# Performance work log

Measured on AMD Instinct MI355X. Metric: run time of the kernel, lower is better.

## Reference

```python
import jax, jax.numpy as jnp
import numpy as np

# ---- constants mirroring init_kwargs ----
S = 128          # sheet_units
KA = 25          # aff_cf_units
C = 2            # aff_cf_channels
KL = 25          # lat_cf_units
EXC = 9          # exc_units
DA = 1           # aff_cf_dilation
DL = 1           # lat_cf_dilation
HOMEO_TARGET = 0.04
STRENGTH = 1.0

# ---- radial helper masks (get_circle / get_radial_cos) ----
def _dist(n):
    g = jnp.arange(n, dtype=jnp.float32) - (n - 1) / 2.0
    return jnp.sqrt(g[:, None] ** 2 + g[None, :] ** 2)

def _circle(n, r):
    return (_dist(n) < r).astype(jnp.float32)

def _rcos(n, wl):
    return jnp.cos(_dist(n) * jnp.pi / wl)

# afferent envelope: [C*KA*KA], channel-major like torch repeat+view
_ae = _rcos(KA, KA) ** 2 * _circle(KA, KA / 2)
_ae = _ae / _ae.max()
AFF_ENV = jnp.tile(_ae.reshape(1, KA * KA), (C, 1)).reshape(C * KA * KA)

# lateral (LRI) envelope: [KL*KL]
_inh = _rcos(KL, EXC / DL) ** 2 * _circle(KL, EXC / (2 * DL))
_le = _rcos(KL, KL) ** 2 * (1.0 - _inh) * _circle(KL, KL / 2)
LRI_ENV = (_le / _le.max()).reshape(KL * KL)

def _unfold(x, k, dil):
    """x: [C,H,W] -> patches [L, C*k*k], torch F.unfold ordering (C slowest)."""
    Cc, H, W = x.shape
    out = H - dil * (k - 1)
    idx = jnp.arange(out)[:, None] + dil * jnp.arange(k)[None, :]  # [out,k]
    p = x[:, idx, :]          # [C,out,k,W]
    p = p[:, :, :, idx]       # [C,out,k,out,k]
    p = p.transpose(1, 3, 0, 2, 4)  # [out_i,out_j,C,ki,kj]
    return p.reshape(out * out, Cc * k * k)

def setup_inputs() -> dict:
    key = jax.random.key(0)
    k1, k2 = jax.random.split(key)
    in_size = S + DA * (KA - 1)  # 152
    x = jax.random.uniform(k1, (1, C, in_size, in_size), dtype=jnp.float32)
    rfs = jax.random.uniform(k2, (S * S, C * KA * KA, 1), dtype=jnp.float32)
    rfs = rfs / rfs.sum(1, keepdims=True)
    lat_weights = jnp.ones((S * S, KL * KL, 1), jnp.float32) / (KL * KL)
    adathresh = jnp.zeros((1, 1, S, S), jnp.float32)
    return {"x": x, "rfs": rfs, "lat_weights": lat_weights, "adathresh": adathresh}

def _forward(x, rfs, lat_weights, adathresh):
    relu = jax.nn.relu
    rfs = relu(rfs)                 # no_grad positive clamp of params
    lw = relu(lat_weights)
    # afferent: unfold + envelope + per-pixel dot (bmm with [L,F,1])
    tiles = _unfold(x[0], KA, DA) * AFF_ENV[None, :]          # [L, C*KA*KA]
    raw_aff = jnp.einsum('lf,lf->l', tiles, rfs[:, :, 0]).reshape(S, S)
    aff = jax.lax.stop_gradient(raw_aff) - adathresh[0, 0]
    lat = relu(aff)
    # lateral inhibition: pad so unfold yields S*S positions
    p = DL * (KL - 1) // 2
    lt = _unfold(jnp.pad(lat, p)[None], KL, DL) * LRI_ENV[None, :]  # [L, KL*KL]
    lat_neg = jnp.einsum('lf,lf->l', lt, jax.lax.stop_gradient(lw)[:, :, 0]).reshape(S, S)
    lat = lat - lat_neg
    lat = jnp.tanh(relu(lat * STRENGTH + aff))
    # hebbian lateral correlations term (learning_flag path)
    lt2 = _unfold(jnp.pad(lat, p, constant_values=HOMEO_TARGET)[None], KL, DL) * LRI_ENV[None, :]
    weighted = lt2 * lat.reshape(S * S, 1)
    lat_correlations = jnp.einsum('lf,lf->', weighted, lw[:, :, 0])
    return (raw_aff.reshape(1, 1, S, S), lat.reshape(1, 1, S, S),
            lat_correlations, tiles[:, None, :])

def reference(x, rfs, lat_weights, adathresh):
    return _forward(x, rfs, lat_weights, adathresh)
```

## Files before the change

kernel.cpp:

```cpp
#include <hip/hip_runtime.h>
#include <math.h>

#define S 128
#define KA 25
#define KL 25
#define PATCH (KA * KA)
#define FEAT (2 * PATCH)
#define PI_F 3.14159265358979323846f

#define WS_ENV 0
#define WS_LAT0 640
#define WS_PART 17024

__global__ __launch_bounds__(256) void k_tiles_aff(const float* __restrict__ x,
                                                   const float* __restrict__ rfs,
                                                   const float* __restrict__ ada,
                                                   float* __restrict__ raw_aff,
                                                   float* __restrict__ tiles,
                                                   float* __restrict__ ws) {
    __shared__ float s_ae[PATCH];
    __shared__ float s_part[4];
    const int tid = threadIdx.x;
    const int lane = tid & 63;
    const int wv = tid >> 6;

    for (int i = tid; i < PATCH; i += 256) {
        float di = (float)(i / KA) - 12.0f;
        float dj = (float)(i % KA) - 12.0f;
        float d = sqrtf(di * di + dj * dj);
        float v = 0.0f;
        if (d < 12.5f) {
            float c = cosf(d * (PI_F / 25.0f));
            v = c * c;
        }
        s_ae[i] = v;
    }
    __syncthreads();

    const int l = blockIdx.x;
    const int li = l >> 7;
    const int lj = l & 127;
    const long base = (long)l * FEAT;

    float acc = 0.0f;
    for (int f = tid; f < FEAT; f += 256) {
        int c = (f >= PATCH) ? 1 : 0;
        int r = f - c * PATCH;
        int ki = r / KA;
        int kj = r - ki * KA;
        float xv = x[c * (152 * 152) + (li + ki) * 152 + (lj + kj)];
        float t = xv * s_ae[r];
        tiles[base + f] = t;
        acc += t * fmaxf(rfs[base + f], 0.0f);
    }

    for (int off = 32; off > 0; off >>= 1) acc += __shfl_down(acc, off);
    if (lane == 0) s_part[wv] = acc;
    __syncthreads();
    if (tid == 0) {
        float ra = s_part[0] + s_part[1] + s_part[2] + s_part[3];
        raw_aff[l] = ra;
        ws[WS_LAT0 + l] = fmaxf(ra - ada[l], 0.0f);
    }

    if (blockIdx.x == 0) {
        __syncthreads();
        float m = 0.0f;
        for (int i = tid; i < PATCH; i += 256) {
            float di = (float)(i / KL) - 12.0f;
            float dj = (float)(i % KL) - 12.0f;
            float d = sqrtf(di * di + dj * dj);
            float v = 0.0f;
            if (d < 12.5f) {
                float c1 = cosf(d * (PI_F / 25.0f));
                float inh = 0.0f;
                if (d < 4.5f) {
                    float c2 = cosf(d * (PI_F / 9.0f));
                    inh = c2 * c2;
                }
                v = c1 * c1 * (1.0f - inh);
            }
            s_ae[i] = v;
            m = fmaxf(m, v);
        }
        for (int off = 32; off > 0; off >>= 1) m = fmaxf(m, __shfl_down(m, off));
        if (lane == 0) s_part[wv] = m;
        __syncthreads();
        float inv = 1.0f / fmaxf(fmaxf(s_part[0], s_part[1]),
                                 fmaxf(s_part[2], s_part[3]));
        for (int i = tid; i < PATCH; i += 256) ws[WS_ENV + i] = s_ae[i] * inv;
    }
}

__global__ __launch_bounds__(256) void k_lat(const float* __restrict__ raw_aff,
                                             const float* __restrict__ ada,
                                             const float* __restrict__ lw,
                                             float* __restrict__ latf,
                                             const float* __restrict__ ws) {
    __shared__ float s_le[PATCH];
    const int tid = threadIdx.x;
    for (int i = tid; i < PATCH; i += 256) s_le[i] = ws[WS_ENV + i];
    __syncthreads();

    const int lane = tid & 63;
    const int wv = tid >> 6;
    const int l = blockIdx.x * 4 + wv;
    const int li = l >> 7;
    const int lj = l & 127;
    const long base = (long)l * PATCH;
    const float* __restrict__ lat0 = ws + WS_LAT0;

    float acc = 0.0f;
    for (int f = lane; f < PATCH; f += 64) {
        int ki = f / KL;
        int kj = f - ki * KL;
        int ri = li + ki - 12;
        int rj = lj + kj - 12;
        float lv = 0.0f;
        if (ri >= 0 && ri < S && rj >= 0 && rj < S) lv = lat0[ri * S + rj];
        acc += lv * s_le[f] * fmaxf(lw[base + f], 0.0f);
    }
    for (int off = 32; off > 0; off >>= 1) acc += __shfl_down(acc, off);

    if (lane == 0) {
        float aff_l = raw_aff[l] - ada[l];
        float lat0_l = fmaxf(aff_l, 0.0f);
        float v = (lat0_l - acc)  + aff_l;
        latf[l] = tanhf(fmaxf(v, 0.0f));
    }
}

__global__ __launch_bounds__(256) void k_corr(const float* __restrict__ latf,
                                              const float* __restrict__ lw,
                                              float* __restrict__ ws) {
    __shared__ float s_le[PATCH];
    __shared__ float s_part[4];
    const int tid = threadIdx.x;
    for (int i = tid; i < PATCH; i += 256) s_le[i] = ws[WS_ENV + i];
    __syncthreads();

    const int lane = tid & 63;
    const int wv = tid >> 6;
    const int l = blockIdx.x * 4 + wv;
    const int li = l >> 7;
    const int lj = l & 127;
    const long base = (long)l * PATCH;

    float acc = 0.0f;
    for (int f = lane; f < PATCH; f += 64) {
        int ki = f / KL;
        int kj = f - ki * KL;
        int ri = li + ki - 12;
        int rj = lj + kj - 12;
        float lv = 0.04f;
        if (ri >= 0 && ri < S && rj >= 0 && rj < S) lv = latf[ri * S + rj];
        acc += lv * s_le[f] * fmaxf(lw[base + f], 0.0f);
    }
    for (int off = 32; off > 0; off >>= 1) acc += __shfl_down(acc, off);

    if (lane == 0) s_part[wv] = acc * latf[l];
    __syncthreads();
    if (tid == 0)
        ws[WS_PART + blockIdx.x] = s_part[0] + s_part[1] + s_part[2] + s_part[3];
}

__global__ __launch_bounds__(256) void k_reduce(const float* __restrict__ ws,
                                                float* __restrict__ corr) {
    __shared__ float s_part[4];
    const int tid = threadIdx.x;
    const int lane = tid & 63;
    const int wv = tid >> 6;
    float acc = 0.0f;
    for (int i = tid; i < 4096; i += 256) acc += ws[WS_PART + i];
    for (int off = 32; off > 0; off >>= 1) acc += __shfl_down(acc, off);
    if (lane == 0) s_part[wv] = acc;
    __syncthreads();
    if (tid == 0) corr[0] = s_part[0] + s_part[1] + s_part[2] + s_part[3];
}

extern "C" void kernel_launch(void* const* d_in, const int* in_sizes, int n_in,
                              void* d_out, int out_size, void* d_ws, size_t ws_size,
                              hipStream_t stream) {
    const float* x   = (const float*)d_in[0];
    const float* rfs = (const float*)d_in[1];
    const float* lw  = (const float*)d_in[2];
    const float* ada = (const float*)d_in[3];

    float* out      = (float*)d_out;
    float* raw_aff  = out;
    float* latf     = out + S * S;
    float* corr     = out + 2 * S * S;
    float* tiles    = out + 2 * S * S + 1;
    float* ws       = (float*)d_ws;

    k_tiles_aff<<<S * S, 256, 0, stream>>>(x, rfs, ada, raw_aff, tiles, ws);
    k_lat<<<(S * S) / 4, 256, 0, stream>>>(raw_aff, ada, lw, latf, ws);
    k_corr<<<(S * S) / 4, 256, 0, stream>>>(latf, lw, ws);
    k_reduce<<<1, 256, 0, stream>>>(ws, corr);
}
```

Measured before the change: 229.1 us.

## Vectorize rfs/tiles/lat-weight accesses with float4 by processing pixel pairs/quads

The afferent kernel now handles two pixels per block so that rfs reads can be float4-aligned. Tile stores are written as float4 through a pointer shifted by one element, because the tiles output starts at an odd offset. The lateral and correlation kernels each give a wavefront four consecutive pixels, so lat_weights are read as aligned float4 and accumulated into four per-pixel sums. This cuts the number of memory instructions on the large streaming arrays, at the cost of extra index arithmetic per element, fewer blocks, and a special-cased final tile element.

```diff
diff --git a/kernel.cpp b/kernel.cpp
--- a/kernel.cpp
+++ b/kernel.cpp
@@ -4,8 +4,8 @@
 #define S 128
 #define KA 25
 #define KL 25
-#define PATCH (KA * KA)
-#define FEAT (2 * PATCH)
+#define PATCH 625
+#define FEAT 1250
 #define PI_F 3.14159265358979323846f
 
 #define WS_ENV 0
@@ -19,7 +19,7 @@
                                                    float* __restrict__ tiles,
                                                    float* __restrict__ ws) {
     __shared__ float s_ae[PATCH];
-    __shared__ float s_part[4];
+    __shared__ float s_part[8];
     const int tid = threadIdx.x;
     const int lane = tid & 63;
     const int wv = tid >> 6;
@@ -29,38 +29,66 @@
         float dj = (float)(i % KA) - 12.0f;
         float d = sqrtf(di * di + dj * dj);
         float v = 0.0f;
-        if (d < 12.5f) {
-            float c = cosf(d * (PI_F / 25.0f));
-            v = c * c;
-        }
+        if (d < 12.5f) { float c = cosf(d * (PI_F / 25.0f)); v = c * c; }
         s_ae[i] = v;
     }
     __syncthreads();
 
-    const int l = blockIdx.x;
-    const int li = l >> 7;
-    const int lj = l & 127;
-    const long base = (long)l * FEAT;
-
-    float acc = 0.0f;
-    for (int f = tid; f < FEAT; f += 256) {
-        int c = (f >= PATCH) ? 1 : 0;
-        int r = f - c * PATCH;
-        int ki = r / KA;
-        int kj = r - ki * KA;
-        float xv = x[c * (152 * 152) + (li + ki) * 152 + (lj + kj)];
-        float t = xv * s_ae[r];
-        tiles[base + f] = t;
-        acc += t * fmaxf(rfs[base + f], 0.0f);
-    }
-
-    for (int off = 32; off > 0; off >>= 1) acc += __shfl_down(acc, off);
-    if (lane == 0) s_part[wv] = acc;
+    const int p = blockIdx.x;
+    const long pbase = (long)p * 2500;
+    const float4* __restrict__ rfs4 = (const float4*)(rfs + pbase);
+    float4* __restrict__ st4 = (float4*)(tiles + pbase - 1);
+
+    float acc0 = 0.0f, acc1 = 0.0f;
+    for (int k = tid; k < 625; k += 256) {
+        float t[5];
+#pragma unroll
+        for (int e = 0; e < 5; ++e) {
+            int fp = 4 * k - 1 + e;
+            int u = fp + 1250;
+            int li_ = u / 1250;
+            int f = u - 1250 * li_;
+            int l = 2 * p + li_ - 1;
+            if (l < 0) l = 0;
+            int c = f >= 625;
+            int r = f - 625 * c;
+            int ki = r / 25;
+            int kj = r - 25 * ki;
+            int li = l >> 7, lj = l & 127;
+            t[e] = x[c * (152 * 152) + (li + ki) * 152 + (lj + kj)] * s_ae[r];
+        }
+        st4[k] = make_float4(t[0], t[1], t[2], t[3]);
+        float4 rv = rfs4[k];
+        if (4 * k + 3 < 1250) {
+            acc0 += t[1] * fmaxf(rv.x, 0.f) + t[2] * fmaxf(rv.y, 0.f)
+                  + t[3] * fmaxf(rv.z, 0.f) + t[4] * fmaxf(rv.w, 0.f);
+        } else if (4 * k >= 1250) {
+            acc1 += t[1] * fmaxf(rv.x, 0.f) + t[2] * fmaxf(rv.y, 0.f)
+                  + t[3] * fmaxf(rv.z, 0.f) + t[4] * fmaxf(rv.w, 0.f);
+        } else {
+            acc0 += t[1] * fmaxf(rv.x, 0.f) + t[2] * fmaxf(rv.y, 0.f);
+            acc1 += t[3] * fmaxf(rv.z, 0.f) + t[4] * fmaxf(rv.w, 0.f);
+        }
+    }
+
+    if (p == 8191 && tid == 0) {
+        tiles[pbase + 2499] = x[152 * 152 + 151 * 152 + 151] * s_ae[624];
+    }
+
+    for (int off = 32; off > 0; off >>= 1) {
+        acc0 += __shfl_down(acc0, off);
+        acc1 += __shfl_down(acc1, off);
+    }
+    if (lane == 0) { s_part[wv] = acc0; s_part[4 + wv] = acc1; }
     __syncthreads();
     if (tid == 0) {
-        float ra = s_part[0] + s_part[1] + s_part[2] + s_part[3];
-        raw_aff[l] = ra;
-        ws[WS_LAT0 + l] = fmaxf(ra - ada[l], 0.0f);
+        float ra0 = s_part[0] + s_part[1] + s_part[2] + s_part[3];
+        float ra1 = s_part[4] + s_part[5] + s_part[6] + s_part[7];
+        int l0 = 2 * p;
+        raw_aff[l0] = ra0;
+        raw_aff[l0 + 1] = ra1;
+        ws[WS_LAT0 + l0] = fmaxf(ra0 - ada[l0], 0.0f);
+        ws[WS_LAT0 + l0 + 1] = fmaxf(ra1 - ada[l0 + 1], 0.0f);
     }
 
     if (blockIdx.x == 0) {
@@ -74,10 +102,7 @@
             if (d < 12.5f) {
                 float c1 = cosf(d * (PI_F / 25.0f));
                 float inh = 0.0f;
-                if (d < 4.5f) {
-                    float c2 = cosf(d * (PI_F / 9.0f));
-                    inh = c2 * c2;
-                }
+                if (d < 4.5f) { float c2 = cosf(d * (PI_F / 9.0f)); inh = c2 * c2; }
                 v = c1 * c1 * (1.0f - inh);
             }
             s_ae[i] = v;
@@ -104,29 +129,47 @@
 
     const int lane = tid & 63;
     const int wv = tid >> 6;
-    const int l = blockIdx.x * 4 + wv;
-    const int li = l >> 7;
-    const int lj = l & 127;
-    const long base = (long)l * PATCH;
+    const int q = blockIdx.x * 4 + wv;
+    const int l0 = q * 4;
+    const float4* __restrict__ lw4 = (const float4*)(lw + (long)q * 2500);
     const float* __restrict__ lat0 = ws + WS_LAT0;
 
-    float acc = 0.0f;
-    for (int f = lane; f < PATCH; f += 64) {
-        int ki = f / KL;
-        int kj = f - ki * KL;
-        int ri = li + ki - 12;
-        int rj = lj + kj - 12;
-        float lv = 0.0f;
-        if (ri >= 0 && ri < S && rj >= 0 && rj < S) lv = lat0[ri * S + rj];
-        acc += lv * s_le[f] * fmaxf(lw[base + f], 0.0f);
-    }
-    for (int off = 32; off > 0; off >>= 1) acc += __shfl_down(acc, off);
-
+    float a0 = 0.f, a1 = 0.f, a2 = 0.f, a3 = 0.f;
+    for (int k = lane; k < 625; k += 64) {
+        float4 w4 = lw4[k];
+        float w[4] = { w4.x, w4.y, w4.z, w4.w };
+#pragma unroll
+        for (int e = 0; e < 4; ++e) {
+            int fp = 4 * k + e;
+            int li_ = fp / 625;
+            int r = fp - 625 * li_;
+            int ki = r / 25;
+            int kj = r - 25 * ki;
+            int l = l0 + li_;
+            int ri = (l >> 7) + ki - 12;
+            int rj = (l & 127) + kj - 12;
+            float lv = 0.0f;
+            if (ri >= 0 && ri < S && rj >= 0 && rj < S) lv = lat0[ri * S + rj];
+            float contrib = lv * s_le[r] * fmaxf(w[e], 0.0f);
+            a0 += (li_ == 0) ? contrib : 0.0f;
+            a1 += (li_ == 1) ? contrib : 0.0f;
+            a2 += (li_ == 2) ? contrib : 0.0f;
+            a3 += (li_ == 3) ? contrib : 0.0f;
+        }
+    }
+    for (int off = 32; off > 0; off >>= 1) {
+        a0 += __shfl_down(a0, off); a1 += __shfl_down(a1, off);
+        a2 += __shfl_down(a2, off); a3 += __shfl_down(a3, off);
+    }
     if (lane == 0) {
-        float aff_l = raw_aff[l] - ada[l];
-        float lat0_l = fmaxf(aff_l, 0.0f);
-        float v = (lat0_l - acc)  + aff_l;
-        latf[l] = tanhf(fmaxf(v, 0.0f));
+        float acc[4] = { a0, a1, a2, a3 };
+#pragma unroll
+        for (int j = 0; j < 4; ++j) {
+            int l = l0 + j;
+            float aff_l = raw_aff[l] - ada[l];
+            float v = fmaxf(aff_l, 0.0f) - acc[j] + aff_l;
+            latf[l] = tanhf(fmaxf(v, 0.0f));
+        }
     }
 }
 
@@ -141,24 +184,41 @@
 
     const int lane = tid & 63;
     const int wv = tid >> 6;
-    const int l = blockIdx.x * 4 + wv;
-    const int li = l >> 7;
-    const int lj = l & 127;
-    const long base = (long)l * PATCH;
-
-    float acc = 0.0f;
-    for (int f = lane; f < PATCH; f += 64) {
-        int ki = f / KL;
-        int kj = f - ki * KL;
-        int ri = li + ki - 12;
-        int rj = lj + kj - 12;
-        float lv = 0.04f;
-        if (ri >= 0 && ri < S && rj >= 0 && rj < S) lv = latf[ri * S + rj];
-        acc += lv * s_le[f] * fmaxf(lw[base + f], 0.0f);
-    }
-    for (int off = 32; off > 0; off >>= 1) acc += __shfl_down(acc, off);
-
-    if (lane == 0) s_part[wv] = acc * latf[l];
+    const int q = blockIdx.x * 4 + wv;
+    const int l0 = q * 4;
+    const float4* __restrict__ lw4 = (const float4*)(lw + (long)q * 2500);
+
+    float a0 = 0.f, a1 = 0.f, a2 = 0.f, a3 = 0.f;
+    for (int k = lane; k < 625; k += 64) {
+        float4 w4 = lw4[k];
+        float w[4] = { w4.x, w4.y, w4.z, w4.w };
+#pragma unroll
+        for (int e = 0; e < 4; ++e) {
+            int fp = 4 * k + e;
+            int li_ = fp / 625;
+            int r = fp - 625 * li_;
+            int ki = r / 25;
+            int kj = r - 25 * ki;
+            int l = l0 + li_;
+            int ri = (l >> 7) + ki - 12;
+            int rj = (l & 127) + kj - 12;
+            float lv = 0.04f;
+            if (ri >= 0 && ri < S && rj >= 0 && rj < S) lv = latf[ri * S + rj];
+            float contrib = lv * s_le[r] * fmaxf(w[e], 0.0f);
+            a0 += (li_ == 0) ? contrib : 0.0f;
+            a1 += (li_ == 1) ? contrib : 0.0f;
+            a2 += (li_ == 2) ? contrib : 0.0f;
+            a3 += (li_ == 3) ? contrib : 0.0f;
+        }
+    }
+    for (int off = 32; off > 0; off >>= 1) {
+        a0 += __shfl_down(a0, off); a1 += __shfl_down(a1, off);
+        a2 += __shfl_down(a2, off); a3 += __shfl_down(a3, off);
+    }
+    if (lane == 0) {
+        s_part[wv] = a0 * latf[l0] + a1 * latf[l0 + 1]
+                   + a2 * latf[l0 + 2] + a3 * latf[l0 + 3];
+    }
     __syncthreads();
     if (tid == 0)
         ws[WS_PART + blockIdx.x] = s_part[0] + s_part[1] + s_part[2] + s_part[3];
@@ -171,7 +231,7 @@
     const int lane = tid & 63;
     const int wv = tid >> 6;
     float acc = 0.0f;
-    for (int i = tid; i < 4096; i += 256) acc += ws[WS_PART + i];
+    for (int i = tid; i < 1024; i += 256) acc += ws[WS_PART + i];
     for (int off = 32; off > 0; off >>= 1) acc += __shfl_down(acc, off);
     if (lane == 0) s_part[wv] = acc;
     __syncthreads();
@@ -193,8 +253,8 @@
     float* tiles    = out + 2 * S * S + 1;
     float* ws       = (float*)d_ws;
 
-    k_tiles_aff<<<S * S, 256, 0, stream>>>(x, rfs, ada, raw_aff, tiles, ws);
-    k_lat<<<(S * S) / 4, 256, 0, stream>>>(raw_aff, ada, lw, latf, ws);
-    k_corr<<<(S * S) / 4, 256, 0, stream>>>(latf, lw, ws);
+    k_tiles_aff<<<(S * S) / 2, 256, 0, stream>>>(x, rfs, ada, raw_aff, tiles, ws);
+    k_lat<<<(S * S) / 16, 256, 0, stream>>>(raw_aff, ada, lw, latf, ws);
+    k_corr<<<(S * S) / 16, 256, 0, stream>>>(latf, lw, ws);
     k_reduce<<<1, 256, 0, stream>>>(ws, corr);
 }
```

After: 232.6 us. No clear change (+1.5%).
